# Kernel tuning notes

Hardware: AMD Instinct MI355X
Metric: run time of the kernel (lower is better)

## Reference

```python
import jax, jax.numpy as jnp
import numpy as np

FEAT = 1024
HID = 512
DK = 256
N = 8192
KMAX = 8
K_LIST = (2, 4, 8)


def setup_inputs() -> dict:
    key = jax.random.key(0)
    ks = jax.random.split(key, 10)
    def glorot(k, shape):
        lim = np.sqrt(6.0 / (shape[0] + shape[1]))
        return jax.random.uniform(k, shape, jnp.float32, -lim, lim)
    return {
        "input_tensor": jax.random.normal(ks[0], (N, FEAT), jnp.float32),
        "sp_matrix": jax.random.randint(ks[1], (N, KMAX + 1), 0, N, jnp.int64 if jax.config.jax_enable_x64 else jnp.int32),
        "W1": glorot(ks[2], (FEAT, HID)),
        "b1": jnp.zeros((HID,), jnp.float32),
        "Wq": glorot(ks[3], (HID, DK)),
        "Wk": glorot(ks[4], (HID, DK)),
        "Wv": glorot(ks[5], (HID, DK)),
        "bv": jnp.zeros((DK,), jnp.float32),
        "Wout": glorot(ks[6], (DK, 2)),
        "bout": jnp.zeros((2,), jnp.float32),
    }


def reference(input_tensor, sp_matrix, W1, b1, Wq, Wk, Wv, bv, Wout, bout):
    # fc1: Dense(512, relu)
    dense = jax.nn.relu(input_tensor @ W1 + b1)            # [n, 512]
    # CustomAttention: scaled QK^T over the whole bag
    q = dense @ Wq                                          # [n, 256]
    k = dense @ Wk                                          # [n, 256]
    attn = (q @ k.T) / jnp.sqrt(jnp.float32(DK))            # [n, n]
    value = dense @ Wv + bv                                 # [n, 256]
    pools = []
    for kk in K_LIST:
        idx = sp_matrix[:, : kk + 1]                        # [n, kk+1]
        # sparse adjacency * attention, row-sum == gather attn[i, idx[i,j]] and sum over j
        a_raw = jnp.take_along_axis(attn, idx, axis=1).sum(axis=1)  # [n]
        alpha = jax.nn.softmax(a_raw)                       # [n]
        pools.append(alpha[:, None] * value)                # [n, 256]
    spp = jnp.concatenate(pools, axis=0)                    # [3n, 256]
    # Last_Sigmoid (subtyping=True): sum-pool -> dense -> softmax
    logits = spp.sum(axis=0, keepdims=True) @ Wout + bout   # [1, 2]
    return jax.nn.softmax(logits, axis=-1)
```

## Files before the change

### kernel.cpp

```cpp
#include <hip/hip_runtime.h>
#include <hip/hip_bf16.h>
#include <math.h>

#define FEAT 1024
#define HID  512
#define DK   256
#define NROWS 8192

typedef __attribute__((ext_vector_type(8))) short short8;
typedef __attribute__((ext_vector_type(4))) float floatx4;

__device__ __forceinline__ unsigned short f2bf(float x) {
    union { float f; unsigned u; } u;
    u.f = x;
    unsigned r = u.u;
    r += 0x7fffu + ((r >> 16) & 1u);
    return (unsigned short)(r >> 16);
}
__device__ __forceinline__ float bf2f(unsigned short x) {
    union { unsigned u; float f; } u;
    u.u = ((unsigned)x) << 16;
    return u.f;
}

__device__ __forceinline__ void gld_lds16(const unsigned short* g, unsigned short* l) {
    __builtin_amdgcn_global_load_lds(
        (__attribute__((address_space(1))) void*)(void*)g,
        (__attribute__((address_space(3))) void*)l,
        16, 0, 0);
}

__global__ __launch_bounds__(256) void cast_bf16(
    const float* __restrict__ in, unsigned short* __restrict__ out, int n4)
{
    int i = blockIdx.x * 256 + threadIdx.x;
    if (i >= n4) return;
    float4 v = ((const float4*)in)[i];
    ushort4 o;
    o.x = f2bf(v.x); o.y = f2bf(v.y); o.z = f2bf(v.z); o.w = f2bf(v.w);
    ((ushort4*)out)[i] = o;
}

__global__ __launch_bounds__(256) void transpose_cast4(
    const float* __restrict__ W1, const float* __restrict__ Wq,
    const float* __restrict__ Wk, const float* __restrict__ Wv,
    unsigned short* __restrict__ W1T, unsigned short* __restrict__ WqT,
    unsigned short* __restrict__ WkT, unsigned short* __restrict__ WvT)
{
    const int z = blockIdx.z;
    const float* in; unsigned short* out; int K, N;
    if (z == 0)      { in = W1; out = W1T; K = FEAT; N = HID; }
    else if (z == 1) { in = Wq; out = WqT; K = HID;  N = DK;  }
    else if (z == 2) { in = Wk; out = WkT; K = HID;  N = DK;  }
    else             { in = Wv; out = WvT; K = HID;  N = DK;  }

    const int n0 = blockIdx.x * 32, k0 = blockIdx.y * 32;
    if (n0 >= N || k0 >= K) return;

    __shared__ float t[32][33];
    const int tx = threadIdx.x, ty = threadIdx.y;
    #pragma unroll
    for (int i = ty; i < 32; i += 8)
        t[i][tx] = in[(size_t)(k0 + i) * N + (n0 + tx)];
    __syncthreads();
    #pragma unroll
    for (int i = ty; i < 32; i += 8)
        out[(size_t)(n0 + i) * K + (k0 + tx)] = f2bf(t[tx][i]);
}

__global__ __launch_bounds__(256) void gemm_mfma(
    const unsigned short* __restrict__ A,
    const unsigned short* __restrict__ BT0, const unsigned short* __restrict__ BT1,
    const unsigned short* __restrict__ BT2,
    const float* __restrict__ bias0, const float* __restrict__ bias1,
    const float* __restrict__ bias2,
    unsigned short* __restrict__ C0, unsigned short* __restrict__ C1,
    unsigned short* __restrict__ C2,
    int N, int K, int relu)
{
    const unsigned short* BT = (blockIdx.z == 0) ? BT0 : (blockIdx.z == 1) ? BT1 : BT2;
    const float* bias        = (blockIdx.z == 0) ? bias0 : (blockIdx.z == 1) ? bias1 : bias2;
    unsigned short* C        = (blockIdx.z == 0) ? C0 : (blockIdx.z == 1) ? C1 : C2;

    __shared__ __align__(16) unsigned short As[64 * 32];
    __shared__ __align__(16) unsigned short Bs[128 * 32];

    const int tid  = threadIdx.x;
    const int lane = tid & 63;
    const int wid  = tid >> 6;
    const int wm = wid >> 1, wn = wid & 1;
    const int m0 = blockIdx.y * 64, n0 = blockIdx.x * 128;

    const int rowA = tid >> 2, gA = tid & 3;
    const int sgA = gA ^ ((rowA >> 1) & 3);
    const unsigned short* Ap = A + (size_t)(m0 + rowA) * K + sgA * 8;

    const int idx0 = tid, idx1 = tid + 256;
    const int rowB0 = idx0 >> 2, gB0 = idx0 & 3;
    const int rowB1 = idx1 >> 2, gB1 = idx1 & 3;
    const int sgB0 = gB0 ^ ((rowB0 >> 1) & 3);
    const int sgB1 = gB1 ^ ((rowB1 >> 1) & 3);
    const unsigned short* Bp0 = BT + (size_t)(n0 + rowB0) * K + sgB0 * 8;
    const unsigned short* Bp1 = BT + (size_t)(n0 + rowB1) * K + sgB1 * 8;

    char* AsB = (char*)As;
    char* BsB = (char*)Bs;
    const int ldsA  = wid * 1024;
    const int ldsB0 = wid * 1024;
    const int ldsB1 = wid * 1024 + 4096;

    const int gr = lane >> 4;
    int aoff[2], boff[4];
    #pragma unroll
    for (int i = 0; i < 2; ++i) {
        int ra = wm * 32 + i * 16 + (lane & 15);
        aoff[i] = ra * 64 + ((gr ^ ((ra >> 1) & 3)) * 16);
    }
    #pragma unroll
    for (int j = 0; j < 4; ++j) {
        int rb = wn * 64 + j * 16 + (lane & 15);
        boff[j] = rb * 64 + ((gr ^ ((rb >> 1) & 3)) * 16);
    }

    floatx4 acc[2][4];
    #pragma unroll
    for (int i = 0; i < 2; ++i)
        #pragma unroll
        for (int j = 0; j < 4; ++j)
            acc[i][j] = (floatx4){0.f, 0.f, 0.f, 0.f};

    for (int kt = 0; kt < K; kt += 32) {
        gld_lds16(Ap  + kt, (unsigned short*)(AsB + ldsA));
        gld_lds16(Bp0 + kt, (unsigned short*)(BsB + ldsB0));
        gld_lds16(Bp1 + kt, (unsigned short*)(BsB + ldsB1));
        __syncthreads();

        short8 af[2], bfr[4];
        #pragma unroll
        for (int i = 0; i < 2; ++i) af[i] = *(const short8*)(AsB + aoff[i]);
        #pragma unroll
        for (int j = 0; j < 4; ++j) bfr[j] = *(const short8*)(BsB + boff[j]);
        #pragma unroll
        for (int i = 0; i < 2; ++i)
            #pragma unroll
            for (int j = 0; j < 4; ++j)
                acc[i][j] = __builtin_amdgcn_mfma_f32_16x16x32_bf16(
                    af[i], bfr[j], acc[i][j], 0, 0, 0);
        __syncthreads();
    }

    #pragma unroll
    for (int i = 0; i < 2; ++i) {
        int rbase = m0 + wm * 32 + i * 16 + (lane >> 4) * 4;
        #pragma unroll
        for (int j = 0; j < 4; ++j) {
            int c = n0 + wn * 64 + j * 16 + (lane & 15);
            float bb = bias ? bias[c] : 0.f;
            #pragma unroll
            for (int r = 0; r < 4; ++r) {
                float v = acc[i][j][r] + bb;
                if (relu) v = fmaxf(v, 0.f);
                C[(size_t)(rbase + r) * N + c] = f2bf(v);
            }
        }
    }
}

__global__ __launch_bounds__(64) void gather_attn(
    const unsigned short* __restrict__ Q, const unsigned short* __restrict__ Kmat,
    const int* __restrict__ sp, float* __restrict__ a_raw)
{
    const int i = blockIdx.x;
    const int lane = threadIdx.x;

    ushort4 qr = *(const ushort4*)(Q + (size_t)i * DK + lane * 4);
    float4 q = make_float4(bf2f(qr.x), bf2f(qr.y), bf2f(qr.z), bf2f(qr.w));
    float4 ks = make_float4(0.f, 0.f, 0.f, 0.f);

    int sel = 0;
    #pragma unroll
    for (int j = 0; j <= 8; ++j) {
        int r = sp[i * 9 + j];
        ushort4 kr = *(const ushort4*)(Kmat + (size_t)r * DK + lane * 4);
        ks.x += bf2f(kr.x); ks.y += bf2f(kr.y);
        ks.z += bf2f(kr.z); ks.w += bf2f(kr.w);
        if (j == 2 || j == 4 || j == 8) {
            float d = q.x * ks.x + q.y * ks.y + q.z * ks.z + q.w * ks.w;
            #pragma unroll
            for (int off = 32; off; off >>= 1) d += __shfl_xor(d, off);
            if (lane == 0) a_raw[sel * NROWS + i] = d * 0.0625f;
            ++sel;
        }
    }
}

__global__ __launch_bounds__(1024) void reduce_max_k(
    const float* __restrict__ a_raw, float* __restrict__ mx,
    float* __restrict__ P, float* __restrict__ Z)
{
    __shared__ float s[1024];
    const int sel = blockIdx.x;
    if (threadIdx.x < DK) P[sel * DK + threadIdx.x] = 0.f;
    if (threadIdx.x == 0) Z[sel] = 0.f;
    float m = -INFINITY;
    for (int i = threadIdx.x; i < NROWS; i += 1024)
        m = fmaxf(m, a_raw[sel * NROWS + i]);
    s[threadIdx.x] = m;
    __syncthreads();
    for (int st = 512; st; st >>= 1) {
        if (threadIdx.x < st) s[threadIdx.x] = fmaxf(s[threadIdx.x], s[threadIdx.x + st]);
        __syncthreads();
    }
    if (threadIdx.x == 0) mx[sel] = s[0];
}

#define RPB 128
__global__ __launch_bounds__(256) void pool_kernel(
    const float* __restrict__ a_raw, const float* __restrict__ mx,
    const unsigned short* __restrict__ V, float* __restrict__ P,
    float* __restrict__ Z)
{
    const int sel = blockIdx.y;
    const int r0 = blockIdx.x * RPB;
    const int t = threadIdx.x;

    __shared__ float e[RPB];
    __shared__ float zs[4];

    const float m = mx[sel];
    float zp = 0.f;
    if (t < RPB) {
        float v = expf(a_raw[sel * NROWS + r0 + t] - m);
        e[t] = v;
        zp = v;
    }
    __syncthreads();

    float acc = 0.f;
    for (int r = 0; r < RPB; ++r)
        acc = fmaf(e[r], bf2f(V[(size_t)(r0 + r) * DK + t]), acc);
    atomicAdd(&P[sel * DK + t], acc);

    #pragma unroll
    for (int off = 32; off; off >>= 1) zp += __shfl_xor(zp, off);
    if ((t & 63) == 0) zs[t >> 6] = zp;
    __syncthreads();
    if (t == 0) atomicAdd(&Z[sel], zs[0] + zs[1] + zs[2] + zs[3]);
}

__global__ __launch_bounds__(256) void final_kernel(
    const float* __restrict__ P, const float* __restrict__ Z,
    const float* __restrict__ Wout, const float* __restrict__ bout,
    float* __restrict__ out)
{
    const int t = threadIdx.x;
    float s = P[t] / Z[0] + P[DK + t] / Z[1] + P[2 * DK + t] / Z[2];
    __shared__ float s0[256], s1[256];
    s0[t] = s * Wout[t * 2 + 0];
    s1[t] = s * Wout[t * 2 + 1];
    __syncthreads();
    for (int st = 128; st; st >>= 1) {
        if (t < st) { s0[t] += s0[t + st]; s1[t] += s1[t + st]; }
        __syncthreads();
    }
    if (t == 0) {
        float a = s0[0] + bout[0], b = s1[0] + bout[1];
        float mm = fmaxf(a, b);
        float ea = expf(a - mm), eb = expf(b - mm);
        float inv = 1.f / (ea + eb);
        out[0] = ea * inv;
        out[1] = eb * inv;
    }
}

extern "C" void kernel_launch(void* const* d_in, const int* in_sizes, int n_in,
                              void* d_out, int out_size, void* d_ws, size_t ws_size,
                              hipStream_t stream)
{
    const float* X    = (const float*)d_in[0];
    const int*   sp   = (const int*)  d_in[1];
    const float* W1   = (const float*)d_in[2];
    const float* b1   = (const float*)d_in[3];
    const float* Wq   = (const float*)d_in[4];
    const float* Wk   = (const float*)d_in[5];
    const float* Wv   = (const float*)d_in[6];
    const float* bv   = (const float*)d_in[7];
    const float* Wout = (const float*)d_in[8];
    const float* bout = (const float*)d_in[9];
    float* out = (float*)d_out;

    char* w = (char*)d_ws;
    unsigned short* dense_b = (unsigned short*)(w);
    unsigned short* W1T     = (unsigned short*)(w +  8388608);
    unsigned short* WqT     = (unsigned short*)(w +  9437184);
    unsigned short* WkT     = (unsigned short*)(w +  9699328);
    unsigned short* WvT     = (unsigned short*)(w +  9961472);
    float* a_raw            = (float*)(w + 10223616);
    float* P                = (float*)(w + 10321920);
    float* Z                = P + 3 * DK;
    float* mx               = Z + 3;
    unsigned short* Qb      = (unsigned short*)(w + 10485760);
    unsigned short* Kb      = (unsigned short*)(w + 14680064);
    unsigned short* Vb      = (unsigned short*)(w + 18874368);
    unsigned short* Xb      = (unsigned short*)(w + 10485760);

    cast_bf16<<<(NROWS * FEAT / 4 + 255) / 256, 256, 0, stream>>>(X, Xb, NROWS * FEAT / 4);
    transpose_cast4<<<dim3(16, 32, 4), dim3(32, 8), 0, stream>>>(
        W1, Wq, Wk, Wv, W1T, WqT, WkT, WvT);

    gemm_mfma<<<dim3(HID / 128, NROWS / 64, 1), 256, 0, stream>>>(
        Xb, W1T, nullptr, nullptr, b1, nullptr, nullptr,
        dense_b, nullptr, nullptr, HID, FEAT, 1);

    gemm_mfma<<<dim3(DK / 128, NROWS / 64, 3), 256, 0, stream>>>(
        dense_b, WqT, WkT, WvT, nullptr, nullptr, bv,
        Qb, Kb, Vb, DK, HID, 0);

    gather_attn<<<NROWS, 64, 0, stream>>>(Qb, Kb, sp, a_raw);
    reduce_max_k<<<3, 1024, 0, stream>>>(a_raw, mx, P, Z);
    pool_kernel<<<dim3(NROWS / RPB, 3, 1), 256, 0, stream>>>(a_raw, mx, Vb, P, Z);
    final_kernel<<<1, 256, 0, stream>>>(P, Z, Wout, bout, out);
}
```

Baseline: 76.54 us.

## Fuse prep kernels, fold max reduction into gather, pool all k at once

```diff
diff --git a/kernel.cpp b/kernel.cpp
--- a/kernel.cpp
+++ b/kernel.cpp
@@ -23,6 +23,14 @@
     return u.f;
 }
 
+__device__ __forceinline__ unsigned fenc(float f) {
+    unsigned b = __float_as_uint(f);
+    return (b & 0x80000000u) ? ~b : (b | 0x80000000u);
+}
+__device__ __forceinline__ float fdec(unsigned u) {
+    return __uint_as_float((u & 0x80000000u) ? (u ^ 0x80000000u) : ~u);
+}
+
 __device__ __forceinline__ void gld_lds16(const unsigned short* g, unsigned short* l) {
     __builtin_amdgcn_global_load_lds(
         (__attribute__((address_space(1))) void*)(void*)g,
@@ -30,42 +38,51 @@
         16, 0, 0);
 }
 
-__global__ __launch_bounds__(256) void cast_bf16(
-    const float* __restrict__ in, unsigned short* __restrict__ out, int n4)
-{
-    int i = blockIdx.x * 256 + threadIdx.x;
-    if (i >= n4) return;
-    float4 v = ((const float4*)in)[i];
-    ushort4 o;
-    o.x = f2bf(v.x); o.y = f2bf(v.y); o.z = f2bf(v.z); o.w = f2bf(v.w);
-    ((ushort4*)out)[i] = o;
-}
-
-__global__ __launch_bounds__(256) void transpose_cast4(
-    const float* __restrict__ W1, const float* __restrict__ Wq,
-    const float* __restrict__ Wk, const float* __restrict__ Wv,
-    unsigned short* __restrict__ W1T, unsigned short* __restrict__ WqT,
-    unsigned short* __restrict__ WkT, unsigned short* __restrict__ WvT)
-{
-    const int z = blockIdx.z;
-    const float* in; unsigned short* out; int K, N;
-    if (z == 0)      { in = W1; out = W1T; K = FEAT; N = HID; }
-    else if (z == 1) { in = Wq; out = WqT; K = HID;  N = DK;  }
-    else if (z == 2) { in = Wk; out = WkT; K = HID;  N = DK;  }
-    else             { in = Wv; out = WvT; K = HID;  N = DK;  }
-
-    const int n0 = blockIdx.x * 32, k0 = blockIdx.y * 32;
-    if (n0 >= N || k0 >= K) return;
-
-    __shared__ float t[32][33];
-    const int tx = threadIdx.x, ty = threadIdx.y;
-    #pragma unroll
-    for (int i = ty; i < 32; i += 8)
-        t[i][tx] = in[(size_t)(k0 + i) * N + (n0 + tx)];
+__global__ __launch_bounds__(256) void prep_kernel(
+    const float* __restrict__ X, const float* __restrict__ W1,
+    const float* __restrict__ Wq, const float* __restrict__ Wk,
+    const float* __restrict__ Wv,
+    unsigned short* __restrict__ Xb, unsigned short* __restrict__ W1T,
+    unsigned short* __restrict__ WqT, unsigned short* __restrict__ WkT,
+    unsigned short* __restrict__ WvT,
+    float* __restrict__ P, float* __restrict__ Z, unsigned* __restrict__ mx_enc)
+{
+    const int b = blockIdx.x;
+    const int tid = threadIdx.x;
+
+    if (b == 0) {
+        for (int i = tid; i < 3 * DK; i += 256) P[i] = 0.f;
+        if (tid < 3) { Z[tid] = 0.f; mx_enc[tid] = 0u; }
+    }
+    if (b < 8192) {
+        int i = b * 256 + tid;
+        float4 v = ((const float4*)X)[i];
+        ushort4 o;
+        o.x = f2bf(v.x); o.y = f2bf(v.y); o.z = f2bf(v.z); o.w = f2bf(v.w);
+        ((ushort4*)Xb)[i] = o;
+        return;
+    }
+    int t = b - 8192;
+    const float* in; unsigned short* outp; int K, N, tn, tk;
+    if (t < 512) {
+        in = W1; outp = W1T; K = FEAT; N = HID; tn = t & 15; tk = t >> 4;
+    } else {
+        t -= 512;
+        int z = t >> 7, r = t & 127;
+        K = HID; N = DK; tn = r & 7; tk = r >> 3;
+        in   = (z == 0) ? Wq  : (z == 1) ? Wk  : Wv;
+        outp = (z == 0) ? WqT : (z == 1) ? WkT : WvT;
+    }
+    __shared__ float tt[32][33];
+    const int tx = tid & 31, ty = tid >> 5;
+    const int n0 = tn * 32, k0 = tk * 32;
+    #pragma unroll
+    for (int i2 = ty; i2 < 32; i2 += 8)
+        tt[i2][tx] = in[(size_t)(k0 + i2) * N + (n0 + tx)];
     __syncthreads();
     #pragma unroll
-    for (int i = ty; i < 32; i += 8)
-        out[(size_t)(n0 + i) * K + (k0 + tx)] = f2bf(t[tx][i]);
+    for (int i2 = ty; i2 < 32; i2 += 8)
+        outp[(size_t)(n0 + i2) * K + (k0 + tx)] = f2bf(tt[tx][i2]);
 }
 
 __global__ __launch_bounds__(256) void gemm_mfma(
@@ -166,86 +183,93 @@
     }
 }
 
-__global__ __launch_bounds__(64) void gather_attn(
+__global__ __launch_bounds__(256) void gather_attn(
     const unsigned short* __restrict__ Q, const unsigned short* __restrict__ Kmat,
-    const int* __restrict__ sp, float* __restrict__ a_raw)
-{
-    const int i = blockIdx.x;
-    const int lane = threadIdx.x;
-
-    ushort4 qr = *(const ushort4*)(Q + (size_t)i * DK + lane * 4);
-    float4 q = make_float4(bf2f(qr.x), bf2f(qr.y), bf2f(qr.z), bf2f(qr.w));
-    float4 ks = make_float4(0.f, 0.f, 0.f, 0.f);
-
-    int sel = 0;
-    #pragma unroll
-    for (int j = 0; j <= 8; ++j) {
-        int r = sp[i * 9 + j];
-        ushort4 kr = *(const ushort4*)(Kmat + (size_t)r * DK + lane * 4);
-        ks.x += bf2f(kr.x); ks.y += bf2f(kr.y);
-        ks.z += bf2f(kr.z); ks.w += bf2f(kr.w);
-        if (j == 2 || j == 4 || j == 8) {
-            float d = q.x * ks.x + q.y * ks.y + q.z * ks.z + q.w * ks.w;
-            #pragma unroll
-            for (int off = 32; off; off >>= 1) d += __shfl_xor(d, off);
-            if (lane == 0) a_raw[sel * NROWS + i] = d * 0.0625f;
-            ++sel;
+    const int* __restrict__ sp, float* __restrict__ a_raw,
+    unsigned* __restrict__ mx_enc)
+{
+    const int lane = threadIdx.x & 63;
+    const int wid  = threadIdx.x >> 6;
+
+    float mloc[3] = {-INFINITY, -INFINITY, -INFINITY};
+
+    #pragma unroll 1
+    for (int tr = 0; tr < 16; ++tr) {
+        const int i = blockIdx.x * 64 + wid * 16 + tr;
+        ushort4 qr = *(const ushort4*)(Q + (size_t)i * DK + lane * 4);
+        float4 q = make_float4(bf2f(qr.x), bf2f(qr.y), bf2f(qr.z), bf2f(qr.w));
+        float4 ks = make_float4(0.f, 0.f, 0.f, 0.f);
+
+        int sel = 0;
+        #pragma unroll
+        for (int j = 0; j <= 8; ++j) {
+            int r = sp[i * 9 + j];
+            ushort4 kr = *(const ushort4*)(Kmat + (size_t)r * DK + lane * 4);
+            ks.x += bf2f(kr.x); ks.y += bf2f(kr.y);
+            ks.z += bf2f(kr.z); ks.w += bf2f(kr.w);
+            if (j == 2 || j == 4 || j == 8) {
+                float d = q.x * ks.x + q.y * ks.y + q.z * ks.z + q.w * ks.w;
+                #pragma unroll
+                for (int off = 32; off; off >>= 1) d += __shfl_xor(d, off);
+                d *= 0.0625f;
+                if (lane == 0) a_raw[sel * NROWS + i] = d;
+                mloc[sel] = fmaxf(mloc[sel], d);
+                ++sel;
+            }
         }
     }
-}
-
-__global__ __launch_bounds__(1024) void reduce_max_k(
-    const float* __restrict__ a_raw, float* __restrict__ mx,
-    float* __restrict__ P, float* __restrict__ Z)
-{
-    __shared__ float s[1024];
-    const int sel = blockIdx.x;
-    if (threadIdx.x < DK) P[sel * DK + threadIdx.x] = 0.f;
-    if (threadIdx.x == 0) Z[sel] = 0.f;
-    float m = -INFINITY;
-    for (int i = threadIdx.x; i < NROWS; i += 1024)
-        m = fmaxf(m, a_raw[sel * NROWS + i]);
-    s[threadIdx.x] = m;
+
+    __shared__ float sm[3][4];
+    if (lane == 0) {
+        sm[0][wid] = mloc[0]; sm[1][wid] = mloc[1]; sm[2][wid] = mloc[2];
+    }
     __syncthreads();
-    for (int st = 512; st; st >>= 1) {
-        if (threadIdx.x < st) s[threadIdx.x] = fmaxf(s[threadIdx.x], s[threadIdx.x + st]);
-        __syncthreads();
-    }
-    if (threadIdx.x == 0) mx[sel] = s[0];
-}
-
-#define RPB 128
+    if (threadIdx.x < 3) {
+        float m = fmaxf(fmaxf(sm[threadIdx.x][0], sm[threadIdx.x][1]),
+                        fmaxf(sm[threadIdx.x][2], sm[threadIdx.x][3]));
+        atomicMax(&mx_enc[threadIdx.x], fenc(m));
+    }
+}
+
+#define RPB 64
 __global__ __launch_bounds__(256) void pool_kernel(
-    const float* __restrict__ a_raw, const float* __restrict__ mx,
+    const float* __restrict__ a_raw, const unsigned* __restrict__ mx_enc,
     const unsigned short* __restrict__ V, float* __restrict__ P,
     float* __restrict__ Z)
 {
-    const int sel = blockIdx.y;
     const int r0 = blockIdx.x * RPB;
     const int t = threadIdx.x;
 
-    __shared__ float e[RPB];
-    __shared__ float zs[4];
-
-    const float m = mx[sel];
-    float zp = 0.f;
+    __shared__ float e[3][RPB];
+    const float m0 = fdec(mx_enc[0]), m1 = fdec(mx_enc[1]), m2 = fdec(mx_enc[2]);
+
+    float z0 = 0.f, z1 = 0.f, z2 = 0.f;
     if (t < RPB) {
-        float v = expf(a_raw[sel * NROWS + r0 + t] - m);
-        e[t] = v;
-        zp = v;
+        z0 = expf(a_raw[0 * NROWS + r0 + t] - m0);
+        z1 = expf(a_raw[1 * NROWS + r0 + t] - m1);
+        z2 = expf(a_raw[2 * NROWS + r0 + t] - m2);
+        e[0][t] = z0; e[1][t] = z1; e[2][t] = z2;
     }
     __syncthreads();
 
-    float acc = 0.f;
-    for (int r = 0; r < RPB; ++r)
-        acc = fmaf(e[r], bf2f(V[(size_t)(r0 + r) * DK + t]), acc);
-    atomicAdd(&P[sel * DK + t], acc);
-
-    #pragma unroll
-    for (int off = 32; off; off >>= 1) zp += __shfl_xor(zp, off);
-    if ((t & 63) == 0) zs[t >> 6] = zp;
-    __syncthreads();
-    if (t == 0) atomicAdd(&Z[sel], zs[0] + zs[1] + zs[2] + zs[3]);
+    float a0 = 0.f, a1 = 0.f, a2 = 0.f;
+    for (int r = 0; r < RPB; ++r) {
+        float v = bf2f(V[(size_t)(r0 + r) * DK + t]);
+        a0 = fmaf(e[0][r], v, a0);
+        a1 = fmaf(e[1][r], v, a1);
+        a2 = fmaf(e[2][r], v, a2);
+    }
+    atomicAdd(&P[0 * DK + t], a0);
+    atomicAdd(&P[1 * DK + t], a1);
+    atomicAdd(&P[2 * DK + t], a2);
+
+    #pragma unroll
+    for (int off = 32; off; off >>= 1) {
+        z0 += __shfl_xor(z0, off); z1 += __shfl_xor(z1, off); z2 += __shfl_xor(z2, off);
+    }
+    if (t < RPB && (t & 63) == 0) {
+        atomicAdd(&Z[0], z0); atomicAdd(&Z[1], z1); atomicAdd(&Z[2], z2);
+    }
 }
 
 __global__ __launch_bounds__(256) void final_kernel(
@@ -298,15 +322,14 @@
     float* a_raw            = (float*)(w + 10223616);
     float* P                = (float*)(w + 10321920);
     float* Z                = P + 3 * DK;
-    float* mx               = Z + 3;
+    unsigned* mx_enc        = (unsigned*)(Z + 3);
     unsigned short* Qb      = (unsigned short*)(w + 10485760);
     unsigned short* Kb      = (unsigned short*)(w + 14680064);
     unsigned short* Vb      = (unsigned short*)(w + 18874368);
     unsigned short* Xb      = (unsigned short*)(w + 10485760);
 
-    cast_bf16<<<(NROWS * FEAT / 4 + 255) / 256, 256, 0, stream>>>(X, Xb, NROWS * FEAT / 4);
-    transpose_cast4<<<dim3(16, 32, 4), dim3(32, 8), 0, stream>>>(
-        W1, Wq, Wk, Wv, W1T, WqT, WkT, WvT);
+    prep_kernel<<<8192 + 512 + 384, 256, 0, stream>>>(
+        X, W1, Wq, Wk, Wv, Xb, W1T, WqT, WkT, WvT, P, Z, mx_enc);
 
     gemm_mfma<<<dim3(HID / 128, NROWS / 64, 1), 256, 0, stream>>>(
         Xb, W1T, nullptr, nullptr, b1, nullptr, nullptr,
@@ -316,8 +339,7 @@
         dense_b, WqT, WkT, WvT, nullptr, nullptr, bv,
         Qb, Kb, Vb, DK, HID, 0);
 
-    gather_attn<<<NROWS, 64, 0, stream>>>(Qb, Kb, sp, a_raw);
-    reduce_max_k<<<3, 1024, 0, stream>>>(a_raw, mx, P, Z);
-    pool_kernel<<<dim3(NROWS / RPB, 3, 1), 256, 0, stream>>>(a_raw, mx, Vb, P, Z);
+    gather_attn<<<NROWS / 64, 256, 0, stream>>>(Qb, Kb, sp, a_raw, mx_enc);
+    pool_kernel<<<NROWS / RPB, 256, 0, stream>>>(a_raw, mx_enc, Vb, P, Z);
     final_kernel<<<1, 256, 0, stream>>>(P, Z, Wout, bout, out);
 }
```

New measurement: 102.1 us. 33.4% more time.
